# Kernel tuning notes

Measured on AMD Instinct MI355X. Metric: run time of the kernel, lower is better.

Reference implementation:

```python
import jax, jax.numpy as jnp
import numpy as np

S = 197      # 'attention_heads' arg, acts as sequence length
D = 768      # embedding_dim
H = 4 * D    # MLP hidden
B = 64
EPS = 1e-5
SCALE = 1.0 / S ** (-0.5)  # faithful to source: equals sqrt(S)


def _ln(x, w, b):
    # LayerNorm over the last two dims (S, D), elementwise affine (S, D)
    mu = jnp.mean(x, axis=(-2, -1), keepdims=True)
    var = jnp.var(x, axis=(-2, -1), keepdims=True)
    return (x - mu) * jax.lax.rsqrt(var + EPS) * w + b


def setup_inputs() -> dict:
    key = jax.random.key(0)
    ks = jax.random.split(key, 16)
    s = 0.02
    return {
        "x": jax.random.normal(ks[0], (B, S, D), jnp.float32),
        "norm1_w": jnp.ones((S, D), jnp.float32),
        "norm1_b": jnp.zeros((S, D), jnp.float32),
        "Wq": jax.random.normal(ks[1], (D, D), jnp.float32) * s,
        "bq": jnp.zeros((D,), jnp.float32),
        "Wk": jax.random.normal(ks[2], (D, D), jnp.float32) * s,
        "bk": jnp.zeros((D,), jnp.float32),
        "Wv": jax.random.normal(ks[3], (D, D), jnp.float32) * s,
        "bv": jnp.zeros((D,), jnp.float32),
        "norm2_w": jnp.ones((S, D), jnp.float32),
        "norm2_b": jnp.zeros((S, D), jnp.float32),
        "W1": jax.random.normal(ks[4], (D, H), jnp.float32) * s,
        "b1": jnp.zeros((H,), jnp.float32),
        "W2": jax.random.normal(ks[5], (H, D), jnp.float32) * s,
        "b2": jnp.zeros((D,), jnp.float32),
    }


def reference(x, norm1_w, norm1_b, Wq, bq, Wk, bk, Wv, bv,
              norm2_w, norm2_b, W1, b1, W2, b2):
    # --- attention block ---
    h = _ln(x, norm1_w, norm1_b)                     # (B, S, D)
    q = jnp.einsum('bsd,de->bse', h, Wq) + bq
    k = jnp.einsum('bsd,de->bse', h, Wk) + bk
    v = jnp.einsum('bsd,de->bse', h, Wv) + bv
    scores = jnp.einsum('bsd,btd->bst', q, k) * SCALE  # (B, S, S)
    attn = jnp.einsum('bst,btd->bsd', jax.nn.softmax(scores, axis=-1), v)
    x = attn + x
    # --- MLP block ---
    h2 = _ln(x, norm2_w, norm2_b)
    hid = jax.nn.gelu(jnp.einsum('bsd,dh->bsh', h2, W1) + b1, approximate=False)
    mlp = jax.nn.gelu(jnp.einsum('bsh,hd->bsd', hid, W2) + b2, approximate=False)
    return mlp + x
```

## Files before the change

kernel.cpp:

```cpp
#include <hip/hip_runtime.h>
#include <math.h>


#define S_LEN 197
#define DIM   768
#define HDIM  3072
#define BATCH 64
#define NT    (BATCH * S_LEN)
#define NTP   12672
#define SD    (S_LEN * DIM)
#define SROWS 208
#define SCOLS 224
#define PROWS 256

typedef __attribute__((ext_vector_type(4))) float  f32x4;
typedef __attribute__((ext_vector_type(8))) short  short8v;
typedef __attribute__((ext_vector_type(4))) short  short4v;
typedef __attribute__((ext_vector_type(4))) unsigned short ushort4v;

__device__ __forceinline__ ushort f2bf(float f) {
  union { float f; unsigned u; } a; a.f = f;
  unsigned u = a.u;
  u += 0x7FFFu + ((u >> 16) & 1u);
  return (ushort)(u >> 16);
}
__device__ __forceinline__ float b2f(ushort h) {
  union { unsigned u; float f; } a; a.u = ((unsigned)h) << 16;
  return a.f;
}
__device__ __forceinline__ float gelu_f(float x) {
  return 0.5f * x * (1.0f + erff(x * 0.7071067811865476f));
}

template<bool SPLIT>
__global__ __launch_bounds__(256) void transp_k(const float* __restrict__ W,
                                                int K, int N,
                                                ushort* __restrict__ Thi,
                                                ushort* __restrict__ Tlo) {
  __shared__ float tile[32][33];
  const int nb = blockIdx.x * 32, kb = blockIdx.y * 32;
  const int tx = threadIdx.x, ty = threadIdx.y;
#pragma unroll
  for (int i = 0; i < 4; ++i)
    tile[ty + i * 8][tx] = W[(size_t)(kb + ty + i * 8) * N + nb + tx];
  __syncthreads();
#pragma unroll
  for (int i = 0; i < 4; ++i) {
    float v = tile[tx][ty + i * 8];
    size_t o = (size_t)(nb + ty + i * 8) * K + kb + tx;
    ushort h = f2bf(v);
    Thi[o] = h;
    if (SPLIT) Tlo[o] = f2bf(v - b2f(h));
  }
}

template<bool SPLIT>
__global__ __launch_bounds__(1024) void ln_k(const float* __restrict__ x,
                                             const float* __restrict__ w,
                                             const float* __restrict__ bb,
                                             ushort* __restrict__ oHi,
                                             ushort* __restrict__ oLo) {
  const int b = blockIdx.x;
  const float4* xv = (const float4*)(x + (size_t)b * SD);
  const int N4 = SD / 4;
  float sum = 0.f, sq = 0.f;
  for (int i = threadIdx.x; i < N4; i += 1024) {
    float4 v = xv[i];
    sum += (v.x + v.y) + (v.z + v.w);
    sq  += (v.x * v.x + v.y * v.y) + (v.z * v.z + v.w * v.w);
  }
#pragma unroll
  for (int off = 32; off > 0; off >>= 1) {
    sum += __shfl_xor(sum, off);
    sq  += __shfl_xor(sq, off);
  }
  __shared__ float s1[16], s2[16];
  __shared__ float sMu, sRs;
  const int wv = threadIdx.x >> 6;
  if ((threadIdx.x & 63) == 0) { s1[wv] = sum; s2[wv] = sq; }
  __syncthreads();
  if (threadIdx.x == 0) {
    float Sm = 0.f, Q = 0.f;
#pragma unroll
    for (int i = 0; i < 16; ++i) { Sm += s1[i]; Q += s2[i]; }
    float mu = Sm / (float)SD;
    float var = Q / (float)SD - mu * mu;
    sMu = mu;
    sRs = 1.0f / sqrtf(var + 1e-5f);
  }
  __syncthreads();
  const float mu = sMu, rs = sRs;
  const float4* wv4 = (const float4*)w;
  const float4* bv4 = (const float4*)bb;
  ushort4v* oH = (ushort4v*)(oHi + (size_t)b * SD);
  ushort4v* oL = SPLIT ? (ushort4v*)(oLo + (size_t)b * SD) : nullptr;
  for (int i = threadIdx.x; i < N4; i += 1024) {
    float4 v = xv[i], W4 = wv4[i], B4 = bv4[i];
    float h0 = (v.x - mu) * rs * W4.x + B4.x;
    float h1 = (v.y - mu) * rs * W4.y + B4.y;
    float h2 = (v.z - mu) * rs * W4.z + B4.z;
    float h3 = (v.w - mu) * rs * W4.w + B4.w;
    ushort4v hh;
    hh[0] = f2bf(h0); hh[1] = f2bf(h1); hh[2] = f2bf(h2); hh[3] = f2bf(h3);
    oH[i] = hh;
    if (SPLIT) {
      ushort4v ll;
      ll[0] = f2bf(h0 - b2f(hh[0]));
      ll[1] = f2bf(h1 - b2f(hh[1]));
      ll[2] = f2bf(h2 - b2f(hh[2]));
      ll[3] = f2bf(h3 - b2f(hh[3]));
      oL[i] = ll;
    }
  }
}

__global__ __launch_bounds__(64) void softmax_k(const float* __restrict__ scores,
                                                ushort* __restrict__ P) {
  const int s = blockIdx.x, b = blockIdx.y;
  const int lane = threadIdx.x;
  const float* row = scores + ((size_t)b * SROWS + s) * SCOLS;
  float v[4];
  float m = -1e30f;
#pragma unroll
  for (int t = 0; t < 4; ++t) {
    int c = lane + t * 64;
    v[t] = (c < S_LEN) ? row[c] : -1e30f;
    m = fmaxf(m, v[t]);
  }
#pragma unroll
  for (int off = 32; off > 0; off >>= 1) m = fmaxf(m, __shfl_xor(m, off));
  float sum = 0.f;
#pragma unroll
  for (int t = 0; t < 4; ++t) {
    int c = lane + t * 64;
    v[t] = (c < S_LEN) ? expf(v[t] - m) : 0.f;
    sum += v[t];
  }
#pragma unroll
  for (int off = 32; off > 0; off >>= 1) sum += __shfl_xor(sum, off);
  const float inv = 1.0f / sum;
  ushort* prow = P + ((size_t)b * PROWS + s) * SCOLS;
#pragma unroll
  for (int t = 0; t < 4; ++t) {
    int c = lane + t * 64;
    if (c < SCOLS) prow[c] = f2bf(v[t] * inv);
  }
}

#define GBM 128
#define GBN 128
#define GBK 32
#define LSTR 56

enum { EPI_QK = 0, EPI_V, EPI_SCORE, EPI_PV, EPI_GELU, EPI_OUT };

struct GemmArgs {
  const ushort* Ahi; const ushort* Alo; size_t sAb; int lda;
  const ushort* Bhi; const ushort* Blo; size_t sBb; int ldb;
  int K; int Mv; int Nv;
  const float* bias;
  const float* resid; size_t sRb; int ldr;
  float scale;
  float* outF; size_t sOb; int ldo;
  ushort* outHi; ushort* outLo;
};

__device__ __forceinline__ short8v load_frag(const ushort* p) {
  union U { short8v v8; struct P4 { short4v a, b; } p4; } f;
  f.p4.a = *(const short4v*)(p);
  f.p4.b = *(const short4v*)(p + 16);
  return f.v8;
}

template<int NPROD, bool TRANSB, int EPI>
__global__ __launch_bounds__(256) void gemm_k(GemmArgs g) {
  const int tid  = threadIdx.x;
  const int lane = tid & 63;
  const int wid  = tid >> 6;
  const int r    = lane & 15;
  const int gg   = lane >> 4;
  const int wrow = wid >> 1;
  const int wcol = wid & 1;
  const int nbase = blockIdx.x * GBN;
  const int mbase = blockIdx.y * GBM;
  const int b     = blockIdx.z;

  const ushort* Ahi = g.Ahi + (size_t)b * g.sAb;
  const ushort* Bhi = g.Bhi + (size_t)b * g.sBb;
  const ushort* Alo = (NPROD == 3) ? (g.Alo + (size_t)b * g.sAb) : (const ushort*)nullptr;
  const ushort* Blo = (NPROD == 3) ? (g.Blo + (size_t)b * g.sBb) : (const ushort*)nullptr;

  __shared__ ushort sm[(NPROD == 3 ? 4 : 2) * GBM * LSTR];
  ushort* sAhi = sm;
  ushort* sBhi = sm + GBM * LSTR;
  ushort* sAlo = (NPROD == 3) ? (sm + 2 * GBM * LSTR) : (ushort*)nullptr;
  ushort* sBlo = (NPROD == 3) ? (sm + 3 * GBM * LSTR) : (ushort*)nullptr;

  f32x4 acc[4][4];
#pragma unroll
  for (int i = 0; i < 4; ++i)
#pragma unroll
    for (int j = 0; j < 4; ++j) {
      acc[i][j][0] = 0.f; acc[i][j][1] = 0.f; acc[i][j][2] = 0.f; acc[i][j][3] = 0.f;
    }

  for (int kk = 0; kk < g.K; kk += GBK) {
    __syncthreads();
#pragma unroll
    for (int rd = 0; rd < 2; ++rd) {
      const int lin = tid * 8 + rd * 2048;
      {
        const int row = lin >> 5, col = lin & 31;
        const size_t go = (size_t)(mbase + row) * g.lda + (kk + col);
        *(short8v*)(sAhi + row * LSTR + col) = *(const short8v*)(Ahi + go);
        if (NPROD == 3)
          *(short8v*)(sAlo + row * LSTR + col) = *(const short8v*)(Alo + go);
      }
      if (!TRANSB) {
        const int row = lin >> 5, col = lin & 31;
        const size_t go = (size_t)(nbase + row) * g.ldb + (kk + col);
        *(short8v*)(sBhi + row * LSTR + col) = *(const short8v*)(Bhi + go);
        if (NPROD == 3)
          *(short8v*)(sBlo + row * LSTR + col) = *(const short8v*)(Blo + go);
      } else {
        const int kr = lin >> 7, nc = lin & 127;
        union { short8v v; ushort u[8]; } t;
        t.v = *(const short8v*)(Bhi + (size_t)(kk + kr) * g.ldb + (nbase + nc));
#pragma unroll
        for (int e = 0; e < 8; ++e)
          sBhi[(nc + e) * LSTR + kr] = t.u[e];
      }
    }
    __syncthreads();

    short8v aH[4], bH[4], aL[4], bL[4];
#pragma unroll
    for (int i = 0; i < 4; ++i) {
      const int off = (wrow * 64 + i * 16 + r) * LSTR + gg * 4;
      aH[i] = load_frag(sAhi + off);
      if (NPROD == 3) aL[i] = load_frag(sAlo + off);
    }
#pragma unroll
    for (int j = 0; j < 4; ++j) {
      const int off = (wcol * 64 + j * 16 + r) * LSTR + gg * 4;
      bH[j] = load_frag(sBhi + off);
      if (NPROD == 3) bL[j] = load_frag(sBlo + off);
    }
#pragma unroll
    for (int i = 0; i < 4; ++i)
#pragma unroll
      for (int j = 0; j < 4; ++j) {
        acc[i][j] = __builtin_amdgcn_mfma_f32_16x16x32_bf16(aH[i], bH[j], acc[i][j], 0, 0, 0);
        if (NPROD == 3) {
          acc[i][j] = __builtin_amdgcn_mfma_f32_16x16x32_bf16(aH[i], bL[j], acc[i][j], 0, 0, 0);
          acc[i][j] = __builtin_amdgcn_mfma_f32_16x16x32_bf16(aL[i], bH[j], acc[i][j], 0, 0, 0);
        }
      }
  }

#pragma unroll
  for (int i = 0; i < 4; ++i)
#pragma unroll
    for (int j = 0; j < 4; ++j)
#pragma unroll
      for (int e = 0; e < 4; ++e) {
        const int row = mbase + wrow * 64 + i * 16 + gg * 4 + e;
        const int col = nbase + wcol * 64 + j * 16 + r;
        float val = acc[i][j][e];
        if (EPI == EPI_QK) {
          val += g.bias[col];
          ushort hi = f2bf(val);
          ushort lo = f2bf(val - b2f(hi));
          size_t o = (size_t)row * g.ldo + col;
          g.outHi[o] = hi; g.outLo[o] = lo;
        } else if (EPI == EPI_V) {
          val += g.bias[col];
          g.outHi[(size_t)row * g.ldo + col] = f2bf(val);
        } else if (EPI == EPI_SCORE) {
          if (row < g.Mv && col < g.Nv)
            (g.outF + (size_t)b * g.sOb)[(size_t)row * g.ldo + col] = val * g.scale;
        } else if (EPI == EPI_PV) {
          if (row < g.Mv) {
            val += (g.resid + (size_t)b * g.sRb)[(size_t)row * g.ldr + col];
            (g.outF + (size_t)b * g.sOb)[(size_t)row * g.ldo + col] = val;
          }
        } else if (EPI == EPI_GELU) {
          val = gelu_f(val + g.bias[col]);
          g.outHi[(size_t)row * g.ldo + col] = f2bf(val);
        } else {
          if (row < g.Mv) {
            val = gelu_f(val + g.bias[col]);
            val += g.resid[(size_t)row * g.ldr + col];
            g.outF[(size_t)row * g.ldo + col] = val;
          }
        }
      }
}

extern "C" void kernel_launch(void* const* d_in, const int* in_sizes, int n_in,
                              void* d_out, int out_size, void* d_ws, size_t ws_size,
                              hipStream_t stream) {
  const float* x   = (const float*)d_in[0];
  const float* n1w = (const float*)d_in[1];
  const float* n1b = (const float*)d_in[2];
  const float* Wq  = (const float*)d_in[3];
  const float* bq  = (const float*)d_in[4];
  const float* Wk  = (const float*)d_in[5];
  const float* bk  = (const float*)d_in[6];
  const float* Wv  = (const float*)d_in[7];
  const float* bv  = (const float*)d_in[8];
  const float* n2w = (const float*)d_in[9];
  const float* n2b = (const float*)d_in[10];
  const float* W1  = (const float*)d_in[11];
  const float* b1  = (const float*)d_in[12];
  const float* W2  = (const float*)d_in[13];
  const float* b2  = (const float*)d_in[14];
  float* out = (float*)d_out;

  char* ws = (char*)d_ws;
  size_t off = 0;
  auto alloc = [&](size_t bytes) -> char* {
    char* p = ws + off;
    off += (bytes + 255) & ~(size_t)255;
    return p;
  };
  const size_t szDD  = (size_t)DIM * DIM * 2;
  const size_t szDH  = (size_t)DIM * HDIM * 2;
  const size_t szAct = (size_t)NTP * DIM * 2;

  ushort* wqtH = (ushort*)alloc(szDD);
  ushort* wqtL = (ushort*)alloc(szDD);
  ushort* wktH = (ushort*)alloc(szDD);
  ushort* wktL = (ushort*)alloc(szDD);
  ushort* wvtH = (ushort*)alloc(szDD);
  ushort* w1tH = (ushort*)alloc(szDH);
  ushort* w2tH = (ushort*)alloc(szDH);
  ushort* hHi  = (ushort*)alloc(szAct);
  ushort* hLo  = (ushort*)alloc(szAct);
  ushort* qHi  = (ushort*)alloc(szAct);
  ushort* qLo  = (ushort*)alloc(szAct);
  ushort* kHi  = (ushort*)alloc(szAct);
  ushort* kLo  = (ushort*)alloc(szAct);
  ushort* vB   = (ushort*)alloc(szAct);
  float*  scoresWs = (float*)alloc((size_t)BATCH * SROWS * SCOLS * 4);
  ushort* pWs      = (ushort*)alloc((size_t)BATCH * PROWS * SCOLS * 2);
  if (off > ws_size) return;

  float*  x2  = (float*)hHi;
  ushort* h2  = vB;
  ushort* hid = qHi;

  const float SCALE_F = 14.035668847618199f;

  dim3 tb(32, 8);
  hipLaunchKernelGGL((transp_k<true >), dim3(DIM / 32, DIM / 32), tb, 0, stream, Wq, DIM, DIM, wqtH, wqtL);
  hipLaunchKernelGGL((transp_k<true >), dim3(DIM / 32, DIM / 32), tb, 0, stream, Wk, DIM, DIM, wktH, wktL);
  hipLaunchKernelGGL((transp_k<false>), dim3(DIM / 32, DIM / 32), tb, 0, stream, Wv, DIM, DIM, wvtH, (ushort*)nullptr);
  hipLaunchKernelGGL((transp_k<false>), dim3(HDIM / 32, DIM / 32), tb, 0, stream, W1, DIM, HDIM, w1tH, (ushort*)nullptr);
  hipLaunchKernelGGL((transp_k<false>), dim3(DIM / 32, HDIM / 32), tb, 0, stream, W2, HDIM, DIM, w2tH, (ushort*)nullptr);

  hipLaunchKernelGGL((ln_k<true>), dim3(BATCH), dim3(1024), 0, stream, x, n1w, n1b, hHi, hLo);

  GemmArgs a;
  const int BIG = 0x40000000;

  a = GemmArgs{};
  a.Ahi = hHi; a.Alo = hLo; a.sAb = 0; a.lda = DIM;
  a.Bhi = wqtH; a.Blo = wqtL; a.sBb = 0; a.ldb = DIM;
  a.K = DIM; a.Mv = BIG; a.Nv = BIG; a.bias = bq; a.scale = 1.f;
  a.outHi = qHi; a.outLo = qLo; a.ldo = DIM;
  hipLaunchKernelGGL((gemm_k<3, false, EPI_QK>), dim3(DIM / GBN, NTP / GBM, 1), dim3(256), 0, stream, a);
  a.Bhi = wktH; a.Blo = wktL; a.bias = bk; a.outHi = kHi; a.outLo = kLo;
  hipLaunchKernelGGL((gemm_k<3, false, EPI_QK>), dim3(DIM / GBN, NTP / GBM, 1), dim3(256), 0, stream, a);
  a = GemmArgs{};
  a.Ahi = hHi; a.sAb = 0; a.lda = DIM;
  a.Bhi = wvtH; a.sBb = 0; a.ldb = DIM;
  a.K = DIM; a.Mv = BIG; a.Nv = BIG; a.bias = bv;
  a.outHi = vB; a.ldo = DIM;
  hipLaunchKernelGGL((gemm_k<1, false, EPI_V>), dim3(DIM / GBN, NTP / GBM, 1), dim3(256), 0, stream, a);

  a = GemmArgs{};
  a.Ahi = qHi; a.Alo = qLo; a.sAb = (size_t)SD; a.lda = DIM;
  a.Bhi = kHi; a.Blo = kLo; a.sBb = (size_t)SD; a.ldb = DIM;
  a.K = DIM; a.Mv = S_LEN; a.Nv = S_LEN; a.scale = SCALE_F;
  a.outF = scoresWs; a.sOb = (size_t)SROWS * SCOLS; a.ldo = SCOLS;
  hipLaunchKernelGGL((gemm_k<3, false, EPI_SCORE>), dim3(2, 2, BATCH), dim3(256), 0, stream, a);

  hipLaunchKernelGGL(softmax_k, dim3(S_LEN, BATCH), dim3(64), 0, stream, scoresWs, pWs);

  a = GemmArgs{};
  a.Ahi = pWs; a.sAb = (size_t)PROWS * SCOLS; a.lda = SCOLS;
  a.Bhi = vB; a.sBb = (size_t)SD; a.ldb = DIM;
  a.K = SCOLS; a.Mv = S_LEN; a.Nv = BIG;
  a.resid = x; a.sRb = (size_t)SD; a.ldr = DIM;
  a.outF = x2; a.sOb = (size_t)SD; a.ldo = DIM;
  hipLaunchKernelGGL((gemm_k<1, true, EPI_PV>), dim3(DIM / GBN, 2, BATCH), dim3(256), 0, stream, a);

  hipLaunchKernelGGL((ln_k<false>), dim3(BATCH), dim3(1024), 0, stream, x2, n2w, n2b, h2, (ushort*)nullptr);

  a = GemmArgs{};
  a.Ahi = h2; a.sAb = 0; a.lda = DIM;
  a.Bhi = w1tH; a.sBb = 0; a.ldb = DIM;
  a.K = DIM; a.Mv = BIG; a.Nv = BIG; a.bias = b1;
  a.outHi = hid; a.ldo = HDIM;
  hipLaunchKernelGGL((gemm_k<1, false, EPI_GELU>), dim3(HDIM / GBN, NTP / GBM, 1), dim3(256), 0, stream, a);

  a = GemmArgs{};
  a.Ahi = hid; a.sAb = 0; a.lda = HDIM;
  a.Bhi = w2tH; a.sBb = 0; a.ldb = HDIM;
  a.K = HDIM; a.Mv = NT; a.Nv = BIG; a.bias = b2;
  a.resid = x2; a.sRb = 0; a.ldr = DIM;
  a.outF = out; a.sOb = 0; a.ldo = DIM;
  hipLaunchKernelGGL((gemm_k<1, false, EPI_OUT>), dim3(DIM / GBN, NTP / GBM, 1), dim3(256), 0, stream, a);
}
```

Baseline: 856.2 us.

## Use direct global-to-LDS loads, BK=64 tiles, XCD-aware block remap, split LayerNorm

GEMM tiles are now loaded with global_load_lds (16-byte direct-to-LDS) into unpadded shared layouts. The K-tile depth becomes a template parameter, set to 64 for the V, MLP1 and MLP2 GEMMs. Workgroup IDs are remapped so neighbouring tiles land on the same XCD, which should improve L2 reuse. LayerNorm is split into partial-sum, finalize and apply kernels so far more than 64 blocks run at once. The unpadded LDS layout (stride BK) may cause bank conflicts on fragment reads, and the extra launches add overhead.

```diff
diff --git a/kernel.cpp b/kernel.cpp
--- a/kernel.cpp
+++ b/kernel.cpp
@@ -31,6 +31,11 @@
 __device__ __forceinline__ float gelu_f(float x) {
   return 0.5f * x * (1.0f + erff(x * 0.7071067811865476f));
 }
+__device__ __forceinline__ void gload16(const void* g, void* l) {
+  __builtin_amdgcn_global_load_lds(
+      (const __attribute__((address_space(1))) void*)g,
+      (__attribute__((address_space(3))) void*)l, 16, 0, 0);
+}
 
 template<bool SPLIT>
 __global__ __launch_bounds__(256) void transp_k(const float* __restrict__ W,
@@ -54,63 +59,74 @@
   }
 }
 
-template<bool SPLIT>
-__global__ __launch_bounds__(1024) void ln_k(const float* __restrict__ x,
-                                             const float* __restrict__ w,
-                                             const float* __restrict__ bb,
-                                             ushort* __restrict__ oHi,
-                                             ushort* __restrict__ oLo) {
-  const int b = blockIdx.x;
+#define LN_CH 4
+__global__ __launch_bounds__(256) void ln_part_k(const float* __restrict__ x,
+                                                 float* __restrict__ pbuf) {
+  const int c = blockIdx.x, b = blockIdx.y;
   const float4* xv = (const float4*)(x + (size_t)b * SD);
-  const int N4 = SD / 4;
+  const int per = (SD / 4) / LN_CH;
   float sum = 0.f, sq = 0.f;
-  for (int i = threadIdx.x; i < N4; i += 1024) {
+  for (int i = c * per + threadIdx.x; i < (c + 1) * per; i += 256) {
     float4 v = xv[i];
     sum += (v.x + v.y) + (v.z + v.w);
     sq  += (v.x * v.x + v.y * v.y) + (v.z * v.z + v.w * v.w);
   }
 #pragma unroll
-  for (int off = 32; off > 0; off >>= 1) {
-    sum += __shfl_xor(sum, off);
-    sq  += __shfl_xor(sq, off);
-  }
-  __shared__ float s1[16], s2[16];
-  __shared__ float sMu, sRs;
-  const int wv = threadIdx.x >> 6;
-  if ((threadIdx.x & 63) == 0) { s1[wv] = sum; s2[wv] = sq; }
+  for (int o = 32; o > 0; o >>= 1) {
+    sum += __shfl_xor(sum, o); sq += __shfl_xor(sq, o);
+  }
+  __shared__ float s1[4], s2[4];
+  if ((threadIdx.x & 63) == 0) { s1[threadIdx.x >> 6] = sum; s2[threadIdx.x >> 6] = sq; }
   __syncthreads();
   if (threadIdx.x == 0) {
-    float Sm = 0.f, Q = 0.f;
-#pragma unroll
-    for (int i = 0; i < 16; ++i) { Sm += s1[i]; Q += s2[i]; }
-    float mu = Sm / (float)SD;
-    float var = Q / (float)SD - mu * mu;
-    sMu = mu;
-    sRs = 1.0f / sqrtf(var + 1e-5f);
-  }
-  __syncthreads();
-  const float mu = sMu, rs = sRs;
-  const float4* wv4 = (const float4*)w;
-  const float4* bv4 = (const float4*)bb;
-  ushort4v* oH = (ushort4v*)(oHi + (size_t)b * SD);
-  ushort4v* oL = SPLIT ? (ushort4v*)(oLo + (size_t)b * SD) : nullptr;
-  for (int i = threadIdx.x; i < N4; i += 1024) {
-    float4 v = xv[i], W4 = wv4[i], B4 = bv4[i];
-    float h0 = (v.x - mu) * rs * W4.x + B4.x;
-    float h1 = (v.y - mu) * rs * W4.y + B4.y;
-    float h2 = (v.z - mu) * rs * W4.z + B4.z;
-    float h3 = (v.w - mu) * rs * W4.w + B4.w;
-    ushort4v hh;
-    hh[0] = f2bf(h0); hh[1] = f2bf(h1); hh[2] = f2bf(h2); hh[3] = f2bf(h3);
-    oH[i] = hh;
-    if (SPLIT) {
-      ushort4v ll;
-      ll[0] = f2bf(h0 - b2f(hh[0]));
-      ll[1] = f2bf(h1 - b2f(hh[1]));
-      ll[2] = f2bf(h2 - b2f(hh[2]));
-      ll[3] = f2bf(h3 - b2f(hh[3]));
-      oL[i] = ll;
-    }
+    pbuf[(b * LN_CH + c) * 2]     = s1[0] + s1[1] + s1[2] + s1[3];
+    pbuf[(b * LN_CH + c) * 2 + 1] = s2[0] + s2[1] + s2[2] + s2[3];
+  }
+}
+
+__global__ __launch_bounds__(64) void ln_fin_k(const float* __restrict__ pbuf,
+                                               float* __restrict__ stats) {
+  const int b = threadIdx.x;
+  float S = 0.f, Q = 0.f;
+#pragma unroll
+  for (int c = 0; c < LN_CH; ++c) {
+    S += pbuf[(b * LN_CH + c) * 2];
+    Q += pbuf[(b * LN_CH + c) * 2 + 1];
+  }
+  const float mu = S / (float)SD;
+  const float var = Q / (float)SD - mu * mu;
+  stats[b * 2] = mu;
+  stats[b * 2 + 1] = 1.0f / sqrtf(var + 1e-5f);
+}
+
+template<bool SPLIT>
+__global__ __launch_bounds__(256) void ln_apply_k(const float* __restrict__ x,
+                                                  const float* __restrict__ w,
+                                                  const float* __restrict__ bb,
+                                                  const float* __restrict__ stats,
+                                                  ushort* __restrict__ oHi,
+                                                  ushort* __restrict__ oLo) {
+  const int b = blockIdx.y;
+  const int i = blockIdx.x * 256 + threadIdx.x;
+  if (i >= SD / 4) return;
+  const float mu = stats[b * 2], rs = stats[b * 2 + 1];
+  float4 v  = ((const float4*)(x + (size_t)b * SD))[i];
+  float4 W4 = ((const float4*)w)[i];
+  float4 B4 = ((const float4*)bb)[i];
+  float h0 = (v.x - mu) * rs * W4.x + B4.x;
+  float h1 = (v.y - mu) * rs * W4.y + B4.y;
+  float h2 = (v.z - mu) * rs * W4.z + B4.z;
+  float h3 = (v.w - mu) * rs * W4.w + B4.w;
+  ushort4v hh;
+  hh[0] = f2bf(h0); hh[1] = f2bf(h1); hh[2] = f2bf(h2); hh[3] = f2bf(h3);
+  ((ushort4v*)(oHi + (size_t)b * SD))[i] = hh;
+  if (SPLIT) {
+    ushort4v ll;
+    ll[0] = f2bf(h0 - b2f(hh[0]));
+    ll[1] = f2bf(h1 - b2f(hh[1]));
+    ll[2] = f2bf(h2 - b2f(hh[2]));
+    ll[3] = f2bf(h3 - b2f(hh[3]));
+    ((ushort4v*)(oLo + (size_t)b * SD))[i] = ll;
   }
 }
 
@@ -149,8 +165,6 @@
 
 #define GBM 128
 #define GBN 128
-#define GBK 32
-#define LSTR 56
 
 enum { EPI_QK = 0, EPI_V, EPI_SCORE, EPI_PV, EPI_GELU, EPI_OUT };
 
@@ -165,6 +179,7 @@
   ushort* outHi; ushort* outLo;
 };
 
+template<int STRIDE>
 __device__ __forceinline__ short8v load_frag(const ushort* p) {
   union U { short8v v8; struct P4 { short4v a, b; } p4; } f;
   f.p4.a = *(const short4v*)(p);
@@ -172,8 +187,19 @@
   return f.v8;
 }
 
-template<int NPROD, bool TRANSB, int EPI>
+template<int NPROD, bool TRANSB, int EPI, int BK>
 __global__ __launch_bounds__(256) void gemm_k(GemmArgs g) {
+  constexpr int KSH  = (BK == 64) ? 6 : 5;
+  constexpr int ASZ  = GBM * BK;
+  constexpr int BSTR = TRANSB ? 44 : BK;
+  constexpr int BSZ  = GBN * BSTR;
+  __shared__ __align__(16) ushort sm[(NPROD == 3) ? (2 * ASZ + 2 * BSZ)
+                                                  : (ASZ + BSZ)];
+  ushort* sAhi = sm;
+  ushort* sBhi = sm + ASZ;
+  ushort* sAlo = sm + ASZ + BSZ;
+  ushort* sBlo = sm + 2 * ASZ + BSZ;
+
   const int tid  = threadIdx.x;
   const int lane = tid & 63;
   const int wid  = tid >> 6;
@@ -181,8 +207,15 @@
   const int gg   = lane >> 4;
   const int wrow = wid >> 1;
   const int wcol = wid & 1;
-  const int nbase = blockIdx.x * GBN;
-  const int mbase = blockIdx.y * GBM;
+
+  const int gx = gridDim.x, gy = gridDim.y;
+  const int nwg = gx * gy;
+  const int orig = blockIdx.x + gx * blockIdx.y;
+  const int qq = nwg >> 3, rr = nwg & 7;
+  const int xcd = orig & 7, idx = orig >> 3;
+  const int wg = (xcd < rr ? xcd * (qq + 1) : rr * (qq + 1) + (xcd - rr) * qq) + idx;
+  const int nbase = (wg % gx) * GBN;
+  const int mbase = (wg / gx) * GBM;
   const int b     = blockIdx.z;
 
   const ushort* Ahi = g.Ahi + (size_t)b * g.sAb;
@@ -190,12 +223,6 @@
   const ushort* Alo = (NPROD == 3) ? (g.Alo + (size_t)b * g.sAb) : (const ushort*)nullptr;
   const ushort* Blo = (NPROD == 3) ? (g.Blo + (size_t)b * g.sBb) : (const ushort*)nullptr;
 
-  __shared__ ushort sm[(NPROD == 3 ? 4 : 2) * GBM * LSTR];
-  ushort* sAhi = sm;
-  ushort* sBhi = sm + GBM * LSTR;
-  ushort* sAlo = (NPROD == 3) ? (sm + 2 * GBM * LSTR) : (ushort*)nullptr;
-  ushort* sBlo = (NPROD == 3) ? (sm + 3 * GBM * LSTR) : (ushort*)nullptr;
-
   f32x4 acc[4][4];
 #pragma unroll
   for (int i = 0; i < 4; ++i)
@@ -204,58 +231,65 @@
       acc[i][j][0] = 0.f; acc[i][j][1] = 0.f; acc[i][j][2] = 0.f; acc[i][j][3] = 0.f;
     }
 
-  for (int kk = 0; kk < g.K; kk += GBK) {
+  const int wvb = wid << 10;
+
+  for (int kk = 0; kk < g.K; kk += BK) {
     __syncthreads();
 #pragma unroll
-    for (int rd = 0; rd < 2; ++rd) {
-      const int lin = tid * 8 + rd * 2048;
-      {
-        const int row = lin >> 5, col = lin & 31;
-        const size_t go = (size_t)(mbase + row) * g.lda + (kk + col);
-        *(short8v*)(sAhi + row * LSTR + col) = *(const short8v*)(Ahi + go);
+    for (int rd = 0; rd < BK / 16; ++rd) {
+      const int elem = rd * 2048 + tid * 8;
+      const int row = elem >> KSH, col = elem & (BK - 1);
+      const size_t gaoff = (size_t)(mbase + row) * g.lda + (kk + col);
+      gload16(Ahi + gaoff, (char*)sAhi + rd * 4096 + wvb);
+      if (NPROD == 3)
+        gload16(Alo + gaoff, (char*)sAlo + rd * 4096 + wvb);
+      if (!TRANSB) {
+        const size_t gboff = (size_t)(nbase + row) * g.ldb + (kk + col);
+        gload16(Bhi + gboff, (char*)sBhi + rd * 4096 + wvb);
         if (NPROD == 3)
-          *(short8v*)(sAlo + row * LSTR + col) = *(const short8v*)(Alo + go);
+          gload16(Blo + gboff, (char*)sBlo + rd * 4096 + wvb);
       }
-      if (!TRANSB) {
-        const int row = lin >> 5, col = lin & 31;
-        const size_t go = (size_t)(nbase + row) * g.ldb + (kk + col);
-        *(short8v*)(sBhi + row * LSTR + col) = *(const short8v*)(Bhi + go);
-        if (NPROD == 3)
-          *(short8v*)(sBlo + row * LSTR + col) = *(const short8v*)(Blo + go);
-      } else {
+    }
+    if (TRANSB) {
+#pragma unroll
+      for (int rd = 0; rd < (BK * 128) / 2048; ++rd) {
+        const int lin = tid * 8 + rd * 2048;
         const int kr = lin >> 7, nc = lin & 127;
         union { short8v v; ushort u[8]; } t;
         t.v = *(const short8v*)(Bhi + (size_t)(kk + kr) * g.ldb + (nbase + nc));
 #pragma unroll
         for (int e = 0; e < 8; ++e)
-          sBhi[(nc + e) * LSTR + kr] = t.u[e];
+          sBhi[(nc + e) * BSTR + kr] = t.u[e];
       }
     }
     __syncthreads();
 
-    short8v aH[4], bH[4], aL[4], bL[4];
-#pragma unroll
-    for (int i = 0; i < 4; ++i) {
-      const int off = (wrow * 64 + i * 16 + r) * LSTR + gg * 4;
-      aH[i] = load_frag(sAhi + off);
-      if (NPROD == 3) aL[i] = load_frag(sAlo + off);
+#pragma unroll
+    for (int kb = 0; kb < BK / 32; ++kb) {
+      short8v aH[4], bH[4], aL[4], bL[4];
+#pragma unroll
+      for (int i = 0; i < 4; ++i) {
+        const int off = (wrow * 64 + i * 16 + r) * BK + kb * 32 + gg * 4;
+        aH[i] = load_frag<BK>(sAhi + off);
+        if (NPROD == 3) aL[i] = load_frag<BK>(sAlo + off);
+      }
+#pragma unroll
+      for (int j = 0; j < 4; ++j) {
+        const int off = (wcol * 64 + j * 16 + r) * BSTR + kb * 32 + gg * 4;
+        bH[j] = load_frag<BSTR>(sBhi + off);
+        if (NPROD == 3) bL[j] = load_frag<BSTR>(sBlo + off);
+      }
+#pragma unroll
+      for (int i = 0; i < 4; ++i)
+#pragma unroll
+        for (int j = 0; j < 4; ++j) {
+          acc[i][j] = __builtin_amdgcn_mfma_f32_16x16x32_bf16(aH[i], bH[j], acc[i][j], 0, 0, 0);
+          if (NPROD == 3) {
+            acc[i][j] = __builtin_amdgcn_mfma_f32_16x16x32_bf16(aH[i], bL[j], acc[i][j], 0, 0, 0);
+            acc[i][j] = __builtin_amdgcn_mfma_f32_16x16x32_bf16(aL[i], bH[j], acc[i][j], 0, 0, 0);
+          }
+        }
     }
-#pragma unroll
-    for (int j = 0; j < 4; ++j) {
-      const int off = (wcol * 64 + j * 16 + r) * LSTR + gg * 4;
-      bH[j] = load_frag(sBhi + off);
-      if (NPROD == 3) bL[j] = load_frag(sBlo + off);
-    }
-#pragma unroll
-    for (int i = 0; i < 4; ++i)
-#pragma unroll
-      for (int j = 0; j < 4; ++j) {
-        acc[i][j] = __builtin_amdgcn_mfma_f32_16x16x32_bf16(aH[i], bH[j], acc[i][j], 0, 0, 0);
-        if (NPROD == 3) {
-          acc[i][j] = __builtin_amdgcn_mfma_f32_16x16x32_bf16(aH[i], bL[j], acc[i][j], 0, 0, 0);
-          acc[i][j] = __builtin_amdgcn_mfma_f32_16x16x32_bf16(aL[i], bH[j], acc[i][j], 0, 0, 0);
-        }
-      }
   }
 
 #pragma unroll
@@ -344,6 +378,8 @@
   ushort* vB   = (ushort*)alloc(szAct);
   float*  scoresWs = (float*)alloc((size_t)BATCH * SROWS * SCOLS * 4);
   ushort* pWs      = (ushort*)alloc((size_t)BATCH * PROWS * SCOLS * 2);
+  float*  lnPart   = (float*)alloc((size_t)BATCH * LN_CH * 2 * 4);
+  float*  lnStats  = (float*)alloc((size_t)BATCH * 2 * 4);
   if (off > ws_size) return;
 
   float*  x2  = (float*)hHi;
@@ -359,7 +395,11 @@
   hipLaunchKernelGGL((transp_k<false>), dim3(HDIM / 32, DIM / 32), tb, 0, stream, W1, DIM, HDIM, w1tH, (ushort*)nullptr);
   hipLaunchKernelGGL((transp_k<false>), dim3(DIM / 32, HDIM / 32), tb, 0, stream, W2, HDIM, DIM, w2tH, (ushort*)nullptr);
 
-  hipLaunchKernelGGL((ln_k<true>), dim3(BATCH), dim3(1024), 0, stream, x, n1w, n1b, hHi, hLo);
+  const int APPLY_BX = (SD / 4 + 255) / 256;
+  hipLaunchKernelGGL(ln_part_k, dim3(LN_CH, BATCH), dim3(256), 0, stream, x, lnPart);
+  hipLaunchKernelGGL(ln_fin_k, dim3(1), dim3(64), 0, stream, lnPart, lnStats);
+  hipLaunchKernelGGL((ln_apply_k<true>), dim3(APPLY_BX, BATCH), dim3(256), 0, stream,
+                     x, n1w, n1b, lnStats, hHi, hLo);
 
   GemmArgs a;
   const int BIG = 0x40000000;
@@ -369,22 +409,22 @@
   a.Bhi = wqtH; a.Blo = wqtL; a.sBb = 0; a.ldb = DIM;
   a.K = DIM; a.Mv = BIG; a.Nv = BIG; a.bias = bq; a.scale = 1.f;
   a.outHi = qHi; a.outLo = qLo; a.ldo = DIM;
-  hipLaunchKernelGGL((gemm_k<3, false, EPI_QK>), dim3(DIM / GBN, NTP / GBM, 1), dim3(256), 0, stream, a);
+  hipLaunchKernelGGL((gemm_k<3, false, EPI_QK, 32>), dim3(DIM / GBN, NTP / GBM, 1), dim3(256), 0, stream, a);
   a.Bhi = wktH; a.Blo = wktL; a.bias = bk; a.outHi = kHi; a.outLo = kLo;
-  hipLaunchKernelGGL((gemm_k<3, false, EPI_QK>), dim3(DIM / GBN, NTP / GBM, 1), dim3(256), 0, stream, a);
+  hipLaunchKernelGGL((gemm_k<3, false, EPI_QK, 32>), dim3(DIM / GBN, NTP / GBM, 1), dim3(256), 0, stream, a);
   a = GemmArgs{};
   a.Ahi = hHi; a.sAb = 0; a.lda = DIM;
   a.Bhi = wvtH; a.sBb = 0; a.ldb = DIM;
   a.K = DIM; a.Mv = BIG; a.Nv = BIG; a.bias = bv;
   a.outHi = vB; a.ldo = DIM;
-  hipLaunchKernelGGL((gemm_k<1, false, EPI_V>), dim3(DIM / GBN, NTP / GBM, 1), dim3(256), 0, stream, a);
+  hipLaunchKernelGGL((gemm_k<1, false, EPI_V, 64>), dim3(DIM / GBN, NTP / GBM, 1), dim3(256), 0, stream, a);
 
   a = GemmArgs{};
   a.Ahi = qHi; a.Alo = qLo; a.sAb = (size_t)SD; a.lda = DIM;
   a.Bhi = kHi; a.Blo = kLo; a.sBb = (size_t)SD; a.ldb = DIM;
   a.K = DIM; a.Mv = S_LEN; a.Nv = S_LEN; a.scale = SCALE_F;
   a.outF = scoresWs; a.sOb = (size_t)SROWS * SCOLS; a.ldo = SCOLS;
-  hipLaunchKernelGGL((gemm_k<3, false, EPI_SCORE>), dim3(2, 2, BATCH), dim3(256), 0, stream, a);
+  hipLaunchKernelGGL((gemm_k<3, false, EPI_SCORE, 32>), dim3(2, 2, BATCH), dim3(256), 0, stream, a);
 
   hipLaunchKernelGGL(softmax_k, dim3(S_LEN, BATCH), dim3(64), 0, stream, scoresWs, pWs);
 
@@ -394,16 +434,19 @@
   a.K = SCOLS; a.Mv = S_LEN; a.Nv = BIG;
   a.resid = x; a.sRb = (size_t)SD; a.ldr = DIM;
   a.outF = x2; a.sOb = (size_t)SD; a.ldo = DIM;
-  hipLaunchKernelGGL((gemm_k<1, true, EPI_PV>), dim3(DIM / GBN, 2, BATCH), dim3(256), 0, stream, a);
-
-  hipLaunchKernelGGL((ln_k<false>), dim3(BATCH), dim3(1024), 0, stream, x2, n2w, n2b, h2, (ushort*)nullptr);
+  hipLaunchKernelGGL((gemm_k<1, true, EPI_PV, 32>), dim3(DIM / GBN, 2, BATCH), dim3(256), 0, stream, a);
+
+  hipLaunchKernelGGL(ln_part_k, dim3(LN_CH, BATCH), dim3(256), 0, stream, x2, lnPart);
+  hipLaunchKernelGGL(ln_fin_k, dim3(1), dim3(64), 0, stream, lnPart, lnStats);
+  hipLaunchKernelGGL((ln_apply_k<false>), dim3(APPLY_BX, BATCH), dim3(256), 0, stream,
+                     x2, n2w, n2b, lnStats, h2, (ushort*)nullptr);
 
   a = GemmArgs{};
   a.Ahi = h2; a.sAb = 0; a.lda = DIM;
   a.Bhi = w1tH; a.sBb = 0; a.ldb = DIM;
   a.K = DIM; a.Mv = BIG; a.Nv = BIG; a.bias = b1;
   a.outHi = hid; a.ldo = HDIM;
-  hipLaunchKernelGGL((gemm_k<1, false, EPI_GELU>), dim3(HDIM / GBN, NTP / GBM, 1), dim3(256), 0, stream, a);
+  hipLaunchKernelGGL((gemm_k<1, false, EPI_GELU, 64>), dim3(HDIM / GBN, NTP / GBM, 1), dim3(256), 0, stream, a);
 
   a = GemmArgs{};
   a.Ahi = hid; a.sAb = 0; a.lda = HDIM;
@@ -411,5 +454,5 @@
   a.K = HDIM; a.Mv = NT; a.Nv = BIG; a.bias = b2;
   a.resid = x2; a.sRb = 0; a.ldr = DIM;
   a.outF = out; a.sOb = 0; a.ldo = DIM;
-  hipLaunchKernelGGL((gemm_k<1, false, EPI_OUT>), dim3(DIM / GBN, NTP / GBM, 1), dim3(256), 0, stream, a);
-}
+  hipLaunchKernelGGL((gemm_k<1, false, EPI_OUT, 64>), dim3(DIM / GBN, NTP / GBM, 1), dim3(256), 0, stream, a);
+}
```

New measurement: 1.742 ms. 103% more time.
